# Performance work log

Measured on AMD Instinct MI355X. Metric: run time of the kernel, lower is better.

Reference implementation:

```python
import jax, jax.numpy as jnp
import numpy as np

COMMITMENT_COST = 0.25


def setup_inputs() -> dict:
    key = jax.random.key(0)
    k1, k2 = jax.random.split(key)
    B, S, D, K = 64, 512, 512, 4096
    inputs = jax.random.normal(k1, (B, S, D), dtype=jnp.float32)
    # codebook initialized uniform(-1/K, 1/K) like the torch module
    codebook = jax.random.uniform(k2, (K, D), dtype=jnp.float32,
                                  minval=-1.0 / K, maxval=1.0 / K)
    return {"inputs": inputs, "codebook": codebook}


def reference(inputs, codebook):
    D = inputs.shape[-1]
    flat = inputs.reshape(-1, D)  # [N, D]
    # squared euclidean distances to every code: [N, K]
    dist = (jnp.sum(flat * flat, axis=1, keepdims=True)
            + jnp.sum(codebook * codebook, axis=1)
            - 2.0 * flat @ codebook.T)
    idx = jnp.argmin(dist, axis=1)  # [N]
    # gather replaces one-hot scatter + matmul (same math)
    quantized = codebook[idx].reshape(inputs.shape)
    commitment_loss = jnp.mean((jax.lax.stop_gradient(quantized) - inputs) ** 2)
    codebook_loss = jnp.mean((quantized - jax.lax.stop_gradient(inputs)) ** 2)
    quantize_loss = COMMITMENT_COST * commitment_loss + codebook_loss
    # straight-through estimator
    quantized_st = inputs + jax.lax.stop_gradient(quantized - inputs)
    encoding_indices = idx.reshape(inputs.shape[:-1])
    return quantized_st, quantize_loss, encoding_indices
```

## Files before the change

kernel.cpp:

```cpp
#include <hip/hip_runtime.h>

#define N_ROWS 32768
#define DIM    512
#define KCODES 4096
#define Q_ELEMS (N_ROWS * DIM)
#define LOSS_OFF Q_ELEMS
#define IDX_OFF (Q_ELEMS + 1)

__global__ void k_cnorm(const float* __restrict__ cb, float* __restrict__ cnorm) {
    int wave = (blockIdx.x * blockDim.x + threadIdx.x) >> 6;
    int lane = threadIdx.x & 63;
    if (wave >= KCODES) return;
    const float4* row = (const float4*)(cb + (size_t)wave * DIM);
    float4 v1 = row[lane];
    float4 v2 = row[lane + 64];
    float s = v1.x*v1.x + v1.y*v1.y + v1.z*v1.z + v1.w*v1.w
            + v2.x*v2.x + v2.y*v2.y + v2.z*v2.z + v2.w*v2.w;
    #pragma unroll
    for (int m = 32; m >= 1; m >>= 1) s += __shfl_xor(s, m);
    if (lane == 0) cnorm[wave] = s;
}

__global__ void k_xnorm(const float* __restrict__ x, float* __restrict__ xnorm) {
    int wave = (blockIdx.x * blockDim.x + threadIdx.x) >> 6;
    int lane = threadIdx.x & 63;
    if (wave >= N_ROWS) return;
    const float4* row = (const float4*)(x + (size_t)wave * DIM);
    float4 v1 = row[lane];
    float4 v2 = row[lane + 64];
    float s = v1.x*v1.x + v1.y*v1.y + v1.z*v1.z + v1.w*v1.w
            + v2.x*v2.x + v2.y*v2.y + v2.z*v2.z + v2.w*v2.w;
    #pragma unroll
    for (int m = 32; m >= 1; m >>= 1) s += __shfl_xor(s, m);
    if (lane == 0) xnorm[wave] = s;
}

#define BM 64
#define BN 128
#define BD 32

__global__ __launch_bounds__(256)
void k_argmin(const float* __restrict__ x, const float* __restrict__ cb,
              const float* __restrict__ cnorm, const float* __restrict__ xnorm,
              int* __restrict__ idx_ws, float* __restrict__ idx_out) {
    __shared__ float xs[BM][BD + 4];
    __shared__ float cs[BD][BN];

    const int tid = threadIdx.x;
    const int ty = tid >> 4;
    const int tx = tid & 15;
    const int r0 = blockIdx.x * BM;

    float xn[4];
    #pragma unroll
    for (int i = 0; i < 4; ++i) xn[i] = xnorm[r0 + ty * 4 + i];

    float best[4];
    int   bidx[4];
    #pragma unroll
    for (int i = 0; i < 4; ++i) { best[i] = 3.4e38f; bidx[i] = 0; }

    for (int kc = 0; kc < KCODES; kc += BN) {
        float acc[4][8];
        #pragma unroll
        for (int i = 0; i < 4; ++i)
            #pragma unroll
            for (int j = 0; j < 8; ++j) acc[i][j] = 0.f;

        for (int dc = 0; dc < DIM; dc += BD) {
            #pragma unroll
            for (int it = 0; it < 2; ++it) {
                int f = tid + it * 256;
                int row = f >> 3;
                int dq  = f & 7;
                float4 v = *(const float4*)(x + (size_t)(r0 + row) * DIM + dc + dq * 4);
                *(float4*)&xs[row][dq * 4] = v;
            }
            #pragma unroll
            for (int it = 0; it < 4; ++it) {
                int k  = tid & 127;
                int dq = (tid >> 7) + it * 2;
                float4 v = *(const float4*)(cb + (size_t)(kc + k) * DIM + dc + dq * 4);
                cs[dq * 4 + 0][k] = v.x;
                cs[dq * 4 + 1][k] = v.y;
                cs[dq * 4 + 2][k] = v.z;
                cs[dq * 4 + 3][k] = v.w;
            }
            __syncthreads();

            #pragma unroll 8
            for (int d = 0; d < BD; ++d) {
                float a[4];
                #pragma unroll
                for (int i = 0; i < 4; ++i) a[i] = xs[ty * 4 + i][d];
                float4 b0 = *(const float4*)&cs[d][tx * 4];
                float4 b1 = *(const float4*)&cs[d][64 + tx * 4];
                #pragma unroll
                for (int i = 0; i < 4; ++i) {
                    acc[i][0] = fmaf(a[i], b0.x, acc[i][0]);
                    acc[i][1] = fmaf(a[i], b0.y, acc[i][1]);
                    acc[i][2] = fmaf(a[i], b0.z, acc[i][2]);
                    acc[i][3] = fmaf(a[i], b0.w, acc[i][3]);
                    acc[i][4] = fmaf(a[i], b1.x, acc[i][4]);
                    acc[i][5] = fmaf(a[i], b1.y, acc[i][5]);
                    acc[i][6] = fmaf(a[i], b1.z, acc[i][6]);
                    acc[i][7] = fmaf(a[i], b1.w, acc[i][7]);
                }
            }
            __syncthreads();
        }

        #pragma unroll
        for (int half = 0; half < 2; ++half) {
            #pragma unroll
            for (int j = 0; j < 4; ++j) {
                int k = kc + half * 64 + tx * 4 + j;
                float cn = cnorm[k];
                #pragma unroll
                for (int i = 0; i < 4; ++i) {
                    float t1 = xn[i] + cn;
                    float tw = 2.0f * acc[i][half * 4 + j];
                    float s  = t1 - tw;
                    if (s < best[i]) { best[i] = s; bidx[i] = k; }
                }
            }
        }
    }

    #pragma unroll
    for (int i = 0; i < 4; ++i) {
        float b = best[i];
        int   ix = bidx[i];
        #pragma unroll
        for (int m = 1; m <= 8; m <<= 1) {
            float ob = __shfl_xor(b, m);
            int   oi = __shfl_xor(ix, m);
            if (ob < b || (ob == b && oi < ix)) { b = ob; ix = oi; }
        }
        if (tx == 0) {
            int row = r0 + ty * 4 + i;
            idx_ws[row] = ix;
            idx_out[row] = (float)ix;
        }
    }
}

__global__ void k_gather(const float* __restrict__ x, const float* __restrict__ cb,
                         const int* __restrict__ idx, float* __restrict__ qout,
                         float* __restrict__ partial) {
    int row  = blockIdx.x * 4 + (threadIdx.x >> 6);
    int lane = threadIdx.x & 63;
    int k = idx[row];
    const float4* crow = (const float4*)(cb + (size_t)k * DIM);
    const float4* xrow = (const float4*)(x + (size_t)row * DIM);
    float4* qrow = (float4*)(qout + (size_t)row * DIM);
    float s = 0.f;
    #pragma unroll
    for (int it = 0; it < 2; ++it) {
        int d4 = lane + it * 64;
        float4 q = crow[d4];
        float4 xi = xrow[d4];
        qrow[d4] = q;
        float dx = q.x - xi.x; s += dx * dx;
        dx = q.y - xi.y; s += dx * dx;
        dx = q.z - xi.z; s += dx * dx;
        dx = q.w - xi.w; s += dx * dx;
    }
    #pragma unroll
    for (int m = 32; m >= 1; m >>= 1) s += __shfl_xor(s, m);
    __shared__ float ws4[4];
    if (lane == 0) ws4[threadIdx.x >> 6] = s;
    __syncthreads();
    if (threadIdx.x == 0)
        partial[blockIdx.x] = (ws4[0] + ws4[1]) + (ws4[2] + ws4[3]);
}

__global__ void k_loss(const float* __restrict__ partial, float* __restrict__ out_loss) {
    int t = threadIdx.x;
    double s = 0.0;
    #pragma unroll 4
    for (int i = 0; i < 32; ++i) s += (double)partial[t * 32 + i];
    #pragma unroll
    for (int m = 32; m >= 1; m >>= 1) s += __shfl_xor(s, m);
    __shared__ double sd[4];
    if ((t & 63) == 0) sd[t >> 6] = s;
    __syncthreads();
    if (t == 0) {
        double tot = (sd[0] + sd[1]) + (sd[2] + sd[3]);
        out_loss[0] = (float)(1.25 * tot / (double)Q_ELEMS);
    }
}

extern "C" void kernel_launch(void* const* d_in, const int* in_sizes, int n_in,
                              void* d_out, int out_size, void* d_ws, size_t ws_size,
                              hipStream_t stream) {
    const float* x  = (const float*)d_in[0];
    const float* cb = (const float*)d_in[1];
    float* out = (float*)d_out;

    float* cnorm = (float*)d_ws;
    float* xnorm = (float*)((char*)d_ws + (size_t)KCODES * 4);
    int*   idxw  = (int*)((char*)d_ws + (size_t)(KCODES + N_ROWS) * 4);
    float* part  = (float*)((char*)d_ws + (size_t)(KCODES + 2 * N_ROWS) * 4);

    k_cnorm<<<KCODES / 4, 256, 0, stream>>>(cb, cnorm);
    k_xnorm<<<N_ROWS / 4, 256, 0, stream>>>(x, xnorm);
    k_argmin<<<N_ROWS / BM, 256, 0, stream>>>(x, cb, cnorm, xnorm, idxw, out + IDX_OFF);
    k_gather<<<N_ROWS / 4, 256, 0, stream>>>(x, cb, idxw, out, part);
    k_loss<<<1, 256, 0, stream>>>(part, out + LOSS_OFF);
}
```

Measured before the change: 1.863 ms.

## Split codebook across two grid halves, prefetch tiles into registers, merge argmin in gather

The argmin kernel now splits the 4096 codes into two halves along a second grid dimension, which doubles the block count to 1024. Each block writes a per-half best value and index, and the gather kernel merges the two candidates before writing the index output. The main loop is flattened and software-pipelined: the next x and codebook tiles are loaded into registers while the current tile is computed, and launch bounds request 4 blocks per CU. In exchange, x tiles are loaded twice, the extra workspace traffic is small, and the occupancy hint may push registers to spill. On exact ties between the halves the lower index is still chosen.

```diff
diff --git a/kernel.cpp b/kernel.cpp
--- a/kernel.cpp
+++ b/kernel.cpp
@@ -3,6 +3,7 @@
 #define N_ROWS 32768
 #define DIM    512
 #define KCODES 4096
+#define KHALF  2048
 #define Q_ELEMS (N_ROWS * DIM)
 #define LOSS_OFF Q_ELEMS
 #define IDX_OFF (Q_ELEMS + 1)
@@ -38,11 +39,12 @@
 #define BM 64
 #define BN 128
 #define BD 32
-
-__global__ __launch_bounds__(256)
+#define NCHUNK ((KHALF / BN) * (DIM / BD))
+
+__global__ __launch_bounds__(256, 4)
 void k_argmin(const float* __restrict__ x, const float* __restrict__ cb,
               const float* __restrict__ cnorm, const float* __restrict__ xnorm,
-              int* __restrict__ idx_ws, float* __restrict__ idx_out) {
+              float* __restrict__ bestv, int* __restrict__ bestk) {
     __shared__ float xs[BM][BD + 4];
     __shared__ float cs[BD][BN];
 
@@ -50,6 +52,12 @@
     const int ty = tid >> 4;
     const int tx = tid & 15;
     const int r0 = blockIdx.x * BM;
+    const int kbase = blockIdx.y * KHALF;
+
+    const int xrow1 = tid >> 3,        xdq1 = tid & 7;
+    const int xrow2 = (tid + 256) >> 3, xdq2 = tid & 7;
+    const int ck = tid & 127;
+    const int cdq0 = (tid >> 7);
 
     float xn[4];
     #pragma unroll
@@ -58,70 +66,98 @@
     float best[4];
     int   bidx[4];
     #pragma unroll
-    for (int i = 0; i < 4; ++i) { best[i] = 3.4e38f; bidx[i] = 0; }
-
-    for (int kc = 0; kc < KCODES; kc += BN) {
-        float acc[4][8];
-        #pragma unroll
-        for (int i = 0; i < 4; ++i)
-            #pragma unroll
-            for (int j = 0; j < 8; ++j) acc[i][j] = 0.f;
-
-        for (int dc = 0; dc < DIM; dc += BD) {
-            #pragma unroll
-            for (int it = 0; it < 2; ++it) {
-                int f = tid + it * 256;
-                int row = f >> 3;
-                int dq  = f & 7;
-                float4 v = *(const float4*)(x + (size_t)(r0 + row) * DIM + dc + dq * 4);
-                *(float4*)&xs[row][dq * 4] = v;
+    for (int i = 0; i < 4; ++i) { best[i] = 3.4e38f; bidx[i] = kbase; }
+
+    float acc[4][8];
+
+    float4 xr0, xr1, cr[4];
+
+    {
+        const int kc = 0, dc = 0;
+        xr0 = *(const float4*)(x + (size_t)(r0 + xrow1) * DIM + dc + xdq1 * 4);
+        xr1 = *(const float4*)(x + (size_t)(r0 + xrow2) * DIM + dc + xdq2 * 4);
+        #pragma unroll
+        for (int it2 = 0; it2 < 4; ++it2) {
+            int dq = cdq0 + it2 * 2;
+            cr[it2] = *(const float4*)(cb + (size_t)(kbase + kc * BN + ck) * DIM + dc + dq * 4);
+        }
+    }
+
+    for (int it = 0; it < NCHUNK; ++it) {
+        const int kc = it >> 4;
+
+        __syncthreads();
+        *(float4*)&xs[xrow1][xdq1 * 4] = xr0;
+        *(float4*)&xs[xrow2][xdq2 * 4] = xr1;
+        #pragma unroll
+        for (int it2 = 0; it2 < 4; ++it2) {
+            int dq = cdq0 + it2 * 2;
+            cs[dq * 4 + 0][ck] = cr[it2].x;
+            cs[dq * 4 + 1][ck] = cr[it2].y;
+            cs[dq * 4 + 2][ck] = cr[it2].z;
+            cs[dq * 4 + 3][ck] = cr[it2].w;
+        }
+        __syncthreads();
+
+        if (it + 1 < NCHUNK) {
+            const int nkc = (it + 1) >> 4;
+            const int ndc = ((it + 1) & 15) * BD;
+            xr0 = *(const float4*)(x + (size_t)(r0 + xrow1) * DIM + ndc + xdq1 * 4);
+            xr1 = *(const float4*)(x + (size_t)(r0 + xrow2) * DIM + ndc + xdq2 * 4);
+            #pragma unroll
+            for (int it2 = 0; it2 < 4; ++it2) {
+                int dq = cdq0 + it2 * 2;
+                cr[it2] = *(const float4*)(cb + (size_t)(kbase + nkc * BN + ck) * DIM + ndc + dq * 4);
             }
-            #pragma unroll
-            for (int it = 0; it < 4; ++it) {
-                int k  = tid & 127;
-                int dq = (tid >> 7) + it * 2;
-                float4 v = *(const float4*)(cb + (size_t)(kc + k) * DIM + dc + dq * 4);
-                cs[dq * 4 + 0][k] = v.x;
-                cs[dq * 4 + 1][k] = v.y;
-                cs[dq * 4 + 2][k] = v.z;
-                cs[dq * 4 + 3][k] = v.w;
-            }
-            __syncthreads();
-
-            #pragma unroll 8
-            for (int d = 0; d < BD; ++d) {
-                float a[4];
+        }
+
+        if ((it & 15) == 0) {
+            #pragma unroll
+            for (int i = 0; i < 4; ++i)
                 #pragma unroll
-                for (int i = 0; i < 4; ++i) a[i] = xs[ty * 4 + i][d];
+                for (int j = 0; j < 8; ++j) acc[i][j] = 0.f;
+        }
+
+        #pragma unroll
+        for (int d4 = 0; d4 < 8; ++d4) {
+            float xa[4][4];
+            #pragma unroll
+            for (int i = 0; i < 4; ++i)
+                *(float4*)&xa[i][0] = *(const float4*)&xs[ty * 4 + i][d4 * 4];
+            #pragma unroll
+            for (int dd = 0; dd < 4; ++dd) {
+                int d = d4 * 4 + dd;
                 float4 b0 = *(const float4*)&cs[d][tx * 4];
                 float4 b1 = *(const float4*)&cs[d][64 + tx * 4];
                 #pragma unroll
                 for (int i = 0; i < 4; ++i) {
-                    acc[i][0] = fmaf(a[i], b0.x, acc[i][0]);
-                    acc[i][1] = fmaf(a[i], b0.y, acc[i][1]);
-                    acc[i][2] = fmaf(a[i], b0.z, acc[i][2]);
-                    acc[i][3] = fmaf(a[i], b0.w, acc[i][3]);
-                    acc[i][4] = fmaf(a[i], b1.x, acc[i][4]);
-                    acc[i][5] = fmaf(a[i], b1.y, acc[i][5]);
-                    acc[i][6] = fmaf(a[i], b1.z, acc[i][6]);
-                    acc[i][7] = fmaf(a[i], b1.w, acc[i][7]);
+                    float a = xa[i][dd];
+                    acc[i][0] = fmaf(a, b0.x, acc[i][0]);
+                    acc[i][1] = fmaf(a, b0.y, acc[i][1]);
+                    acc[i][2] = fmaf(a, b0.z, acc[i][2]);
+                    acc[i][3] = fmaf(a, b0.w, acc[i][3]);
+                    acc[i][4] = fmaf(a, b1.x, acc[i][4]);
+                    acc[i][5] = fmaf(a, b1.y, acc[i][5]);
+                    acc[i][6] = fmaf(a, b1.z, acc[i][6]);
+                    acc[i][7] = fmaf(a, b1.w, acc[i][7]);
                 }
             }
-            __syncthreads();
-        }
-
-        #pragma unroll
-        for (int half = 0; half < 2; ++half) {
-            #pragma unroll
-            for (int j = 0; j < 4; ++j) {
-                int k = kc + half * 64 + tx * 4 + j;
-                float cn = cnorm[k];
+        }
+
+        if ((it & 15) == 15) {
+            #pragma unroll
+            for (int half = 0; half < 2; ++half) {
                 #pragma unroll
-                for (int i = 0; i < 4; ++i) {
-                    float t1 = xn[i] + cn;
-                    float tw = 2.0f * acc[i][half * 4 + j];
-                    float s  = t1 - tw;
-                    if (s < best[i]) { best[i] = s; bidx[i] = k; }
+                for (int j = 0; j < 4; ++j) {
+                    int k = kbase + kc * BN + half * 64 + tx * 4 + j;
+                    float cn = cnorm[k];
+                    #pragma unroll
+                    for (int i = 0; i < 4; ++i) {
+                        float t1 = xn[i] + cn;
+                        float tw = 2.0f * acc[i][half * 4 + j];
+                        float s  = t1 - tw;
+                        if (s < best[i]) { best[i] = s; bidx[i] = k; }
+                    }
                 }
             }
         }
@@ -139,18 +175,21 @@
         }
         if (tx == 0) {
             int row = r0 + ty * 4 + i;
-            idx_ws[row] = ix;
-            idx_out[row] = (float)ix;
+            bestv[(size_t)blockIdx.y * N_ROWS + row] = b;
+            bestk[(size_t)blockIdx.y * N_ROWS + row] = ix;
         }
     }
 }
 
 __global__ void k_gather(const float* __restrict__ x, const float* __restrict__ cb,
-                         const int* __restrict__ idx, float* __restrict__ qout,
+                         const float* __restrict__ bestv, const int* __restrict__ bestk,
+                         float* __restrict__ qout, float* __restrict__ idx_out,
                          float* __restrict__ partial) {
     int row  = blockIdx.x * 4 + (threadIdx.x >> 6);
     int lane = threadIdx.x & 63;
-    int k = idx[row];
+    float v0 = bestv[row], v1 = bestv[N_ROWS + row];
+    int   k  = (v1 < v0) ? bestk[N_ROWS + row] : bestk[row];
+    if (lane == 0) idx_out[row] = (float)k;
     const float4* crow = (const float4*)(cb + (size_t)k * DIM);
     const float4* xrow = (const float4*)(x + (size_t)row * DIM);
     float4* qrow = (float4*)(qout + (size_t)row * DIM);
@@ -198,14 +237,17 @@
     const float* cb = (const float*)d_in[1];
     float* out = (float*)d_out;
 
-    float* cnorm = (float*)d_ws;
-    float* xnorm = (float*)((char*)d_ws + (size_t)KCODES * 4);
-    int*   idxw  = (int*)((char*)d_ws + (size_t)(KCODES + N_ROWS) * 4);
-    float* part  = (float*)((char*)d_ws + (size_t)(KCODES + 2 * N_ROWS) * 4);
+    char* ws = (char*)d_ws;
+    float* cnorm = (float*)ws;                      ws += (size_t)KCODES * 4;
+    float* xnorm = (float*)ws;                      ws += (size_t)N_ROWS * 4;
+    float* bestv = (float*)ws;                      ws += (size_t)2 * N_ROWS * 4;
+    int*   bestk = (int*)ws;                        ws += (size_t)2 * N_ROWS * 4;
+    float* part  = (float*)ws;
 
     k_cnorm<<<KCODES / 4, 256, 0, stream>>>(cb, cnorm);
     k_xnorm<<<N_ROWS / 4, 256, 0, stream>>>(x, xnorm);
-    k_argmin<<<N_ROWS / BM, 256, 0, stream>>>(x, cb, cnorm, xnorm, idxw, out + IDX_OFF);
-    k_gather<<<N_ROWS / 4, 256, 0, stream>>>(x, cb, idxw, out, part);
+    dim3 agrid(N_ROWS / BM, 2);
+    k_argmin<<<agrid, 256, 0, stream>>>(x, cb, cnorm, xnorm, bestv, bestk);
+    k_gather<<<N_ROWS / 4, 256, 0, stream>>>(x, cb, bestv, bestk, out, out + IDX_OFF, part);
     k_loss<<<1, 256, 0, stream>>>(part, out + LOSS_OFF);
 }
```

Result: slower. 2.908 ms (+56.1%).
